# Performance work log

Measured on AMD Instinct MI355X. Metric: run time of the kernel, lower is better.

The kernel has to match this reference:

```python
import jax, jax.numpy as jnp
import numpy as np

H = 16  # num_heads
B, N, M, D = 4, 512, 2048, 1024
FF = 4096  # mlp_ratio * D
LN_EPS = 1e-5


def _ln(x, g, b):
    m = x.mean(-1, keepdims=True)
    v = ((x - m) ** 2).mean(-1, keepdims=True)
    return (x - m) * jax.lax.rsqrt(v + LN_EPS) * g + b


def _attn(q_in, k_in, v_in, wq, bq, wk, bk, wv, bv, wp, bp):
    b, n, d = q_in.shape
    m = k_in.shape[1]
    hd = d // H
    scale = hd ** -0.5
    q = (q_in @ wq + bq).reshape(b, n, H, hd) * scale
    k = (k_in @ wk + bk).reshape(b, m, H, hd)
    v = (v_in @ wv + bv).reshape(b, m, H, hd)
    attn = jax.nn.softmax(jnp.einsum('bnhd,bmhd->bhnm', q, k), axis=-1)
    out = jnp.einsum('bhnm,bmhd->bnhd', attn, v).reshape(b, n, d)
    return out @ wp + bp


def setup_inputs() -> dict:
    key = jax.random.key(0)
    ks = iter(jax.random.split(key, 32))
    rnd = lambda shape: jax.random.normal(next(ks), shape, dtype=jnp.float32)
    w = lambda *shape: rnd(shape) * 0.02
    inp = {
        'state': rnd((B, N, D)),
        'patches': rnd((B, M, D)),
        'patches_pos_embed': rnd((B, M, D)),
        'state_query': rnd((B, N, D)),
    }
    for p in ('ca', 'sa'):
        inp[f'{p}_wq'] = w(D, D); inp[f'{p}_bq'] = jnp.zeros((D,), jnp.float32)
        inp[f'{p}_wk'] = w(D, D); inp[f'{p}_bk'] = jnp.zeros((D,), jnp.float32)
        inp[f'{p}_wv'] = w(D, D); inp[f'{p}_bv'] = jnp.zeros((D,), jnp.float32)
        inp[f'{p}_wp'] = w(D, D); inp[f'{p}_bp'] = jnp.zeros((D,), jnp.float32)
    inp['w1'] = w(D, FF); inp['b1'] = jnp.zeros((FF,), jnp.float32)
    inp['w2'] = w(FF, D); inp['b2'] = jnp.zeros((D,), jnp.float32)
    for i in (1, 2, 3):
        inp[f'n{i}_g'] = jnp.ones((D,), jnp.float32)
        inp[f'n{i}_b'] = jnp.zeros((D,), jnp.float32)
        inp[f'ls{i}'] = jnp.full((D,), 1e-5, jnp.float32)
    return inp


def reference(state, patches, patches_pos_embed, state_query,
              ca_wq, ca_bq, ca_wk, ca_bk, ca_wv, ca_bv, ca_wp, ca_bp,
              sa_wq, sa_bq, sa_wk, sa_bk, sa_wv, sa_bv, sa_wp, sa_bp,
              w1, b1, w2, b2,
              n1_g, n1_b, n2_g, n2_b, n3_g, n3_b,
              ls1, ls2, ls3):
    # pre-norm path of TransformerLayer.forward_pre (dropouts/drop_path = 0)
    state = state + state_query
    kv = patches + patches_pos_embed
    cross = _attn(_ln(state, n1_g, n1_b), kv, patches,
                  ca_wq, ca_bq, ca_wk, ca_bk, ca_wv, ca_bv, ca_wp, ca_bp)
    state = state + cross * ls1
    ns = _ln(state, n2_g, n2_b)
    selfa = _attn(ns, ns, ns,
                  sa_wq, sa_bq, sa_wk, sa_bk, sa_wv, sa_bv, sa_wp, sa_bp)
    state = state + selfa * ls2
    h = jax.nn.gelu(_ln(state, n3_g, n3_b) @ w1 + b1)
    return state + (h @ w2 + b2) * ls3
```

## Files before the change

### kernel.cpp

```cpp
#include <hip/hip_runtime.h>

#define DEV __device__ __forceinline__

typedef __bf16 bf16x8 __attribute__((ext_vector_type(8)));
typedef float f32x4 __attribute__((ext_vector_type(4)));

DEV unsigned short f2bf(float f) {
  __bf16 h = (__bf16)f;
  return __builtin_bit_cast(unsigned short, h);
}
DEV unsigned int cvtpk(float lo, float hi) {
  unsigned int r;
  asm("v_cvt_pk_bf16_f32 %0, %1, %2" : "=v"(r) : "v"(lo), "v"(hi));
  return r;
}

DEV void gload16(const void* g, void* l) {
  __builtin_amdgcn_global_load_lds(
      (const __attribute__((address_space(1))) unsigned int*)g,
      (__attribute__((address_space(3))) unsigned int*)l, 16, 0, 0);
}

DEV void tconv64_body(const float* __restrict__ W, unsigned short* __restrict__ Wt,
                      int K, int N, int bx, int by) {
  __shared__ float tile[64][65];
  const int t = threadIdx.x;
  const int rr = t >> 4;
  const int cc = (t & 15) * 4;
#pragma unroll
  for (int it = 0; it < 4; it++) {
    float4 v = *reinterpret_cast<const float4*>(
        &W[(size_t)(by * 64 + it * 16 + rr) * N + bx * 64 + cc]);
    tile[it * 16 + rr][cc] = v.x;
    tile[it * 16 + rr][cc + 1] = v.y;
    tile[it * 16 + rr][cc + 2] = v.z;
    tile[it * 16 + rr][cc + 3] = v.w;
  }
  __syncthreads();
  const int nr = t >> 3;
  const int kc = (t & 7) * 8;
#pragma unroll
  for (int it = 0; it < 2; it++) {
    const int n = it * 32 + nr;
    uint4 o;
    o.x = cvtpk(tile[kc + 0][n], tile[kc + 1][n]);
    o.y = cvtpk(tile[kc + 2][n], tile[kc + 3][n]);
    o.z = cvtpk(tile[kc + 4][n], tile[kc + 5][n]);
    o.w = cvtpk(tile[kc + 6][n], tile[kc + 7][n]);
    *reinterpret_cast<uint4*>(&Wt[(size_t)(bx * 64 + n) * K + by * 64 + kc]) = o;
  }
}

DEV void add_ln_body(const float* __restrict__ a, const float* b, float* x0_out,
                     unsigned short* __restrict__ y, const float* __restrict__ gam,
                     const float* __restrict__ bet, int row) {
  const int t = threadIdx.x;
  const int c = t * 4;
  const size_t base = (size_t)row * 1024 + c;
  float4 v = *reinterpret_cast<const float4*>(a + base);
  if (b) {
    float4 v2 = *reinterpret_cast<const float4*>(b + base);
    v.x += v2.x; v.y += v2.y; v.z += v2.z; v.w += v2.w;
  }
  if (x0_out) *reinterpret_cast<float4*>(x0_out + base) = v;
  float s = v.x + v.y + v.z + v.w;
  float sq = v.x * v.x + v.y * v.y + v.z * v.z + v.w * v.w;
#pragma unroll
  for (int o = 32; o > 0; o >>= 1) {
    s += __shfl_xor(s, o);
    sq += __shfl_xor(sq, o);
  }
  __shared__ float ps[4], pq[4];
  const int w = t >> 6;
  if ((t & 63) == 0) { ps[w] = s; pq[w] = sq; }
  __syncthreads();
  s = ps[0] + ps[1] + ps[2] + ps[3];
  sq = pq[0] + pq[1] + pq[2] + pq[3];
  const float mean = s * (1.f / 1024.f);
  const float var = sq * (1.f / 1024.f) - mean * mean;
  const float rstd = rsqrtf(var + 1e-5f);
  float4 gv = *reinterpret_cast<const float4*>(gam + c);
  float4 bv = *reinterpret_cast<const float4*>(bet + c);
  uint2 o2;
  o2.x = cvtpk((v.x - mean) * rstd * gv.x + bv.x, (v.y - mean) * rstd * gv.y + bv.y);
  o2.y = cvtpk((v.z - mean) * rstd * gv.z + bv.z, (v.w - mean) * rstd * gv.w + bv.w);
  *reinterpret_cast<uint2*>(y + base) = o2;
}

DEV void kvcast_body4(const float* __restrict__ p, const float* __restrict__ pe,
                      unsigned short* __restrict__ kvo, unsigned short* __restrict__ po,
                      int bid) {
  float4 a[4], b[4];
  size_t idx[4];
#pragma unroll
  for (int it = 0; it < 4; it++) {
    idx[it] = ((size_t)bid * 256 + threadIdx.x + (size_t)it * 524288) * 4;
    a[it] = *reinterpret_cast<const float4*>(p + idx[it]);
    b[it] = *reinterpret_cast<const float4*>(pe + idx[it]);
  }
#pragma unroll
  for (int it = 0; it < 4; it++) {
    uint2 kv2, p2;
    kv2.x = cvtpk(a[it].x + b[it].x, a[it].y + b[it].y);
    kv2.y = cvtpk(a[it].z + b[it].z, a[it].w + b[it].w);
    p2.x = cvtpk(a[it].x, a[it].y);
    p2.y = cvtpk(a[it].z, a[it].w);
    *reinterpret_cast<uint2*>(kvo + idx[it]) = kv2;
    *reinterpret_cast<uint2*>(po + idx[it]) = p2;
  }
}

struct Pre {
  const float* sqw[8]; unsigned short* sqd[8];
  const float* w1; unsigned short* w1t;
  const float* w2; unsigned short* w2t;
  const float* state; const float* squery; float* stateF; unsigned short* lnB;
  const float* n1_g; const float* n1_b;
  const float* patches; const float* ppe; unsigned short* kvB; unsigned short* patB;
  const float* bq; const float* bk; const float* bv; float* bqkv;
};
__global__ __launch_bounds__(256) void prelude_kernel(Pre p) {
  const int bid = blockIdx.x;
  if (bid < 2048) {
    kvcast_body4(p.patches, p.ppe, p.kvB, p.patB, bid);
  } else if (bid < 4096) {
    const int i = bid - 2048;
    const int m = i >> 8, wi = i & 255;
    tconv64_body(p.sqw[m], p.sqd[m], 1024, 1024, wi & 15, wi >> 4);
  } else if (bid < 5120) {
    const int i = bid - 4096;
    tconv64_body(p.w1, p.w1t, 1024, 4096, i & 63, i >> 6);
  } else if (bid < 6144) {
    const int i = bid - 5120;
    tconv64_body(p.w2, p.w2t, 4096, 1024, i & 15, i >> 4);
  } else if (bid < 8192) {
    add_ln_body(p.state, p.squery, p.stateF, p.lnB, p.n1_g, p.n1_b, bid - 6144);
  } else {
    const int i = (bid - 8192) * 256 + threadIdx.x;
    p.bqkv[i] = i < 1024 ? p.bq[i] : (i < 2048 ? p.bk[i - 1024] : p.bv[i - 2048]);
  }
}

__global__ __launch_bounds__(256) void add_ln_kernel(
    const float* __restrict__ a, const float* b, float* x0_out,
    unsigned short* __restrict__ y, const float* __restrict__ gam,
    const float* __restrict__ bet) {
  add_ln_body(a, b, x0_out, y, gam, bet, blockIdx.x);
}

DEV void xcd_swizzle(int gx, int gy, int& bx, int& by, int& bz) {
  const int gxy = gx * gy;
  const int nwg = gxy * gridDim.z;
  const int orig = (blockIdx.z * gy + blockIdx.y) * gx + blockIdx.x;
  const int q = nwg >> 3, r = nwg & 7;
  const int xcd = orig & 7;
  int wgid = (xcd < r ? xcd * (q + 1) : r * (q + 1) + (xcd - r) * q) + (orig >> 3);
  bz = wgid / gxy;
  wgid -= bz * gxy;
  if (gy >= gx) { by = wgid / gx; bx = wgid - by * gx; }
  else          { bx = wgid / gy; by = wgid - bx * gy; }
}

template <int BM, int BN>
DEV void gemm_core(const unsigned short* __restrict__ A,
                   const unsigned short* __restrict__ Bt,
                   unsigned short* As, unsigned short* Bs,
                   int brow, int bcol, int K, int lda, int koff,
                   f32x4 (&acc)[BM / 32][BN / 32]) {
  constexpr int WM = BM / 32, WN = BN / 32;
  const int t = threadIdx.x;
  const int lane = t & 63, w = t >> 6;
  const int wr = w >> 1, wc = w & 1;
  const int g = lane >> 4, lr = lane & 15;
  const int srow = lane >> 2, scol = (lane & 3) * 8;

  auto stage = [&](int buf, int k0) {
#pragma unroll
    for (int i = 0; i < BM / 64; i++) {
      const int r0 = (i * 4 + w) * 16;
      gload16(A + (size_t)(brow + r0 + srow) * lda + koff + k0 + scol,
              &As[buf * BM * 32 + r0 * 32]);
    }
#pragma unroll
    for (int i = 0; i < BN / 64; i++) {
      const int r0 = (i * 4 + w) * 16;
      gload16(Bt + (size_t)(bcol + r0 + srow) * lda + koff + k0 + scol,
              &Bs[buf * BN * 32 + r0 * 32]);
    }
  };

  stage(0, 0);
  const int nk = K / 32;
  int cur = 0;
  for (int kt = 0; kt < nk; kt++) {
    __syncthreads();
    if (kt + 1 < nk) stage(cur ^ 1, (kt + 1) * 32);
    bf16x8 af[WM], bfr[WN];
#pragma unroll
    for (int m = 0; m < WM; m++)
      af[m] = *reinterpret_cast<const bf16x8*>(
          &As[cur * BM * 32 + (wr * (BM / 2) + m * 16 + lr) * 32 + g * 8]);
#pragma unroll
    for (int n = 0; n < WN; n++)
      bfr[n] = *reinterpret_cast<const bf16x8*>(
          &Bs[cur * BN * 32 + (wc * (BN / 2) + n * 16 + lr) * 32 + g * 8]);
    __builtin_amdgcn_s_setprio(1);
#pragma unroll
    for (int m = 0; m < WM; m++)
#pragma unroll
      for (int n = 0; n < WN; n++)
        acc[m][n] = __builtin_amdgcn_mfma_f32_16x16x32_bf16(af[m], bfr[n], acc[m][n], 0, 0, 0);
    __builtin_amdgcn_s_setprio(0);
    cur ^= 1;
  }
}

template <int BM, int BN>
DEV void epilogue_vT(f32x4 (&acc)[BM / 32][BN / 32], unsigned short* smem,
                     unsigned short* __restrict__ vT, const float* __restrict__ bias,
                     int brow, int bcol, int vcol0, int vNk, int rpb) {
  constexpr int WM = BM / 32, WN = BN / 32;
  constexpr int LDT = 136;
  const int t = threadIdx.x, lane = t & 63, w = t >> 6;
  const int wr = w >> 1, wc = w & 1;
  const int g = lane >> 4, lr = lane & 15;
  __syncthreads();
#pragma unroll
  for (int m = 0; m < WM; m++) {
    const int row0 = wr * (BM / 2) + m * 16 + g * 4;
#pragma unroll
    for (int n = 0; n < WN; n++) {
      const int cc = wc * (BN / 2) + n * 16 + lr;
      const float bv = bias[bcol + cc];
      uint2 pk;
      pk.x = cvtpk(acc[m][n][0] + bv, acc[m][n][1] + bv);
      pk.y = cvtpk(acc[m][n][2] + bv, acc[m][n][3] + bv);
      *reinterpret_cast<uint2*>(&smem[cc * LDT + row0]) = pk;
    }
  }
  __syncthreads();
  const int b = brow / rpb;
  const int kvb = brow % rpb;
  constexpr int ITERS = BM * BN / (256 * 8);
#pragma unroll
  for (int it = 0; it < ITERS; it++) {
    const int idx = it * 256 + t;
    const int cc = idx / (BM / 8);
    const int ch = idx % (BM / 8);
    const int dg = bcol + cc - vcol0;
    const int h = dg >> 6, d = dg & 63;
    uint4 v = *reinterpret_cast<uint4*>(&smem[cc * LDT + ch * 8]);
    *reinterpret_cast<uint4*>(
        &vT[((size_t)(b * 16 + h) * 64 + d) * vNk + kvb + ch * 8]) = v;
  }
}

template <int EPI, int BM, int BN>
__global__ __launch_bounds__(256) void gemm_kernel(
    const unsigned short* __restrict__ A, const unsigned short* __restrict__ Bt,
    const float* __restrict__ bias, const float* resid,
    const float* __restrict__ ls, void* outp, int M, int N, int K, int lda,
    unsigned short* vT, int vcol0, int vNk, int rpb) {
  constexpr int WM = BM / 32;
  constexpr int WN = BN / 32;
  constexpr int STG = 2 * BM * 32 + 2 * BN * 32;
  constexpr int TRN = BN * 136;
  constexpr int SME = (EPI == 5 && TRN > STG) ? TRN : STG;
  __shared__ __align__(16) unsigned short smem[SME];
  unsigned short* As = smem;
  unsigned short* Bs = smem + 2 * BM * 32;
  const int t = threadIdx.x;
  const int lane = t & 63, w = t >> 6;
  const int wr = w >> 1, wc = w & 1;
  const int g = lane >> 4, lr = lane & 15;

  int bx, by, bz;
  xcd_swizzle(gridDim.x, gridDim.y, bx, by, bz);
  const int brow = by * BM, bcol = bx * BN;

  f32x4 acc[WM][WN] = {};
  gemm_core<BM, BN>(A, Bt, As, Bs, brow, bcol, K, lda, bz * K, acc);

  if (EPI == 5 && bcol >= vcol0) {
    epilogue_vT<BM, BN>(acc, smem, vT, bias, brow, bcol, vcol0, vNk, rpb);
    return;
  }

#pragma unroll
  for (int m = 0; m < WM; m++) {
    const int row0 = brow + wr * (BM / 2) + m * 16 + g * 4;
#pragma unroll
    for (int n = 0; n < WN; n++) {
      const int col = bcol + wc * (BN / 2) + n * 16 + lr;
      const float bv = (EPI == 4) ? 0.f : bias[col];
#pragma unroll
      for (int r = 0; r < 4; r++) {
        const float v = acc[m][n][r] + bv;
        const size_t idx = (size_t)(row0 + r) * N + col;
        if (EPI == 0 || EPI == 5) {
          ((unsigned short*)outp)[idx] = f2bf(v);
        } else if (EPI == 2) {
          ((float*)outp)[idx] = resid[idx] + v * ls[col];
        } else if (EPI == 3) {
          const float tth = tanhf(0.7978845608028654f * (v + 0.044715f * v * v * v));
          ((unsigned short*)outp)[idx] = f2bf(0.5f * v * (1.f + tth));
        } else {
          ((float*)outp)[(size_t)bz * M * N + idx] = v;
        }
      }
    }
  }
}

struct G3 {
  const unsigned short* A[3]; const unsigned short* Bt[3];
  const float* bias[3]; unsigned short* out[3]; int ecum[3];
  unsigned short* vT; int vNk; int rpb;
};
__global__ __launch_bounds__(256) void gemm3_kernel(G3 p, int N, int K) {
  constexpr int BM = 128, BN = 128, WM = BM / 32, WN = BN / 32;
  constexpr int STG = 2 * BM * 32 + 2 * BN * 32;
  constexpr int TRN = BN * 136;
  constexpr int SME = (TRN > STG) ? TRN : STG;
  __shared__ __align__(16) unsigned short smem[SME];
  unsigned short* As = smem;
  unsigned short* Bs = smem + 2 * BM * 32;
  const int t = threadIdx.x;
  const int lane = t & 63, w = t >> 6;
  const int wr = w >> 1, wc = w & 1;
  const int g = lane >> 4, lr = lane & 15;

  int bx, by, bz;
  xcd_swizzle(gridDim.x, gridDim.y, bx, by, bz);
  const int s = (by >= p.ecum[0]) + (by >= p.ecum[1]);
  const int byloc = by - (s ? p.ecum[s - 1] : 0);
  const unsigned short* A = p.A[s];
  const unsigned short* Bt = p.Bt[s];
  const float* bias = p.bias[s];
  const int brow = byloc * BM, bcol = bx * BN;

  f32x4 acc[WM][WN] = {};
  gemm_core<BM, BN>(A, Bt, As, Bs, brow, bcol, K, K, 0, acc);

  if (s == 2) {
    epilogue_vT<BM, BN>(acc, smem, p.vT, bias, brow, bcol, 0, p.vNk, p.rpb);
    return;
  }
  unsigned short* outp = p.out[s];
#pragma unroll
  for (int m = 0; m < WM; m++) {
    const int row0 = brow + wr * (BM / 2) + m * 16 + g * 4;
#pragma unroll
    for (int n = 0; n < WN; n++) {
      const int col = bcol + wc * (BN / 2) + n * 16 + lr;
      const float bv = bias[col];
#pragma unroll
      for (int r = 0; r < 4; r++)
        outp[(size_t)(row0 + r) * N + col] = f2bf(acc[m][n][r] + bv);
    }
  }
}

__global__ __launch_bounds__(256) void splitk_red_kernel(
    const float* __restrict__ p, const float* __restrict__ bias,
    const float* __restrict__ resid, const float* __restrict__ ls,
    float* __restrict__ out) {
  const size_t i = ((size_t)blockIdx.x * 256 + threadIdx.x) * 4;
  const int c = (int)(i & 1023);
  float4 a = *reinterpret_cast<const float4*>(p + i);
  float4 b = *reinterpret_cast<const float4*>(p + 2048ull * 1024 + i);
  float4 rv = *reinterpret_cast<const float4*>(resid + i);
  float4 bb = *reinterpret_cast<const float4*>(bias + c);
  float4 lv = *reinterpret_cast<const float4*>(ls + c);
  float4 o;
  o.x = rv.x + (a.x + b.x + bb.x) * lv.x;
  o.y = rv.y + (a.y + b.y + bb.y) * lv.y;
  o.z = rv.z + (a.z + b.z + bb.z) * lv.z;
  o.w = rv.w + (a.w + b.w + bb.w) * lv.w;
  *reinterpret_cast<float4*>(out + i) = o;
}

__global__ __launch_bounds__(512) void attn_kernel(
    const unsigned short* __restrict__ Q, const unsigned short* __restrict__ Kp,
    const unsigned short* __restrict__ vT, unsigned short* __restrict__ O,
    int RSq, int RSk, int Nq, int Nk, float k2) {
  __shared__ __align__(16) unsigned short Ks[2][128 * 72];
  __shared__ __align__(16) unsigned short Vs[64 * 136];
  __shared__ __align__(16) unsigned short Ps[128 * 72];
  const int t = threadIdx.x, lane = t & 63, w = t >> 6;
  const int qt = blockIdx.y, h = blockIdx.x & 15, b = blockIdx.x >> 4;
  const int g = lane >> 4, lr = lane & 15;
  const int ksrow = t >> 2, kscol = (t & 3) * 16;
  const int vsrow = t >> 3, vscol = (t & 7) * 16;

  uint4 qr[2];
  {
    const unsigned short* qp = Q + (size_t)(b * Nq + qt * 128 + w * 16 + lr) * RSq + h * 64 + g * 8;
    qr[0] = *reinterpret_cast<const uint4*>(qp);
    qr[1] = *reinterpret_cast<const uint4*>(qp + 32);
  }
  float m_i = -1e30f, l_i = 0.f;
  f32x4 acc_o[4] = {};

  auto kaddr = [&](int kv0) {
    return reinterpret_cast<const uint4*>(
        Kp + (size_t)(b * Nk + kv0 + ksrow) * RSk + h * 64 + kscol);
  };
  auto vaddr = [&](int kv0) {
    return reinterpret_cast<const uint4*>(
        vT + ((size_t)(b * 16 + h) * 64 + vsrow) * Nk + kv0 + vscol);
  };

  uint4 kr0 = kaddr(0)[0], kr1 = kaddr(0)[1];
  uint4 vr0 = vaddr(0)[0], vr1 = vaddr(0)[1];

  int cur = 0;
  for (int kv0 = 0; kv0 < Nk; kv0 += 128) {
    *reinterpret_cast<uint4*>(&Ks[cur][ksrow * 72 + kscol]) = kr0;
    *reinterpret_cast<uint4*>(&Ks[cur][ksrow * 72 + kscol + 8]) = kr1;
    *reinterpret_cast<uint4*>(&Vs[vsrow * 136 + vscol]) = vr0;
    *reinterpret_cast<uint4*>(&Vs[vsrow * 136 + vscol + 8]) = vr1;
    __syncthreads();
    if (kv0 + 128 < Nk) {
      kr0 = kaddr(kv0 + 128)[0]; kr1 = kaddr(kv0 + 128)[1];
      vr0 = vaddr(kv0 + 128)[0]; vr1 = vaddr(kv0 + 128)[1];
    }

    f32x4 accs[8] = {};
    __builtin_amdgcn_s_setprio(1);
#pragma unroll
    for (int d0 = 0; d0 < 64; d0 += 32) {
      bf16x8 qf = __builtin_bit_cast(bf16x8, qr[d0 >> 5]);
#pragma unroll
      for (int m = 0; m < 8; m++) {
        bf16x8 kf = *reinterpret_cast<const bf16x8*>(&Ks[cur][(m * 16 + lr) * 72 + d0 + g * 8]);
        accs[m] = __builtin_amdgcn_mfma_f32_16x16x32_bf16(kf, qf, accs[m], 0, 0, 0);
      }
    }
    __builtin_amdgcn_s_setprio(0);
    float pmax = -1e30f;
#pragma unroll
    for (int m = 0; m < 8; m++)
#pragma unroll
      for (int r = 0; r < 4; r++) pmax = fmaxf(pmax, accs[m][r]);
    pmax = fmaxf(pmax, __shfl_xor(pmax, 16));
    pmax = fmaxf(pmax, __shfl_xor(pmax, 32));
    const float pm2 = pmax * k2;
    if (!__all(pm2 <= m_i + 8.f)) {
      const float m_new = fmaxf(m_i, pm2);
      const float corr = exp2f(m_i - m_new);
      m_i = m_new;
      l_i *= corr;
#pragma unroll
      for (int r = 0; r < 4; r++) {
        const float cf = __shfl(corr, g * 4 + r);
#pragma unroll
        for (int n = 0; n < 4; n++) acc_o[n][r] *= cf;
      }
    }
    float psum = 0.f;
    uint2 pk4[4];
#pragma unroll
    for (int m = 0; m < 8; m++) {
      float p0 = exp2f(fmaf(accs[m][0], k2, -m_i));
      float p1 = exp2f(fmaf(accs[m][1], k2, -m_i));
      float p2 = exp2f(fmaf(accs[m][2], k2, -m_i));
      float p3 = exp2f(fmaf(accs[m][3], k2, -m_i));
      psum += p0 + p1 + p2 + p3;
      uint2 pk;
      pk.x = cvtpk(p0, p1);
      pk.y = cvtpk(p2, p3);
      if (m < 4)
        *reinterpret_cast<uint2*>(&Ps[(w * 16 + lr) * 72 + m * 16 + g * 4]) = pk;
      else
        pk4[m - 4] = pk;
    }
    psum += __shfl_xor(psum, 16);
    psum += __shfl_xor(psum, 32);
    l_i += psum;
    __builtin_amdgcn_s_setprio(1);
#pragma unroll
    for (int ks = 0; ks < 2; ks++) {
      bf16x8 pf = *reinterpret_cast<const bf16x8*>(&Ps[(w * 16 + lr) * 72 + ks * 32 + g * 8]);
#pragma unroll
      for (int n = 0; n < 4; n++) {
        bf16x8 vf = *reinterpret_cast<const bf16x8*>(&Vs[(n * 16 + lr) * 136 + ks * 32 + g * 8]);
        acc_o[n] = __builtin_amdgcn_mfma_f32_16x16x32_bf16(pf, vf, acc_o[n], 0, 0, 0);
      }
    }
    __builtin_amdgcn_s_setprio(0);
#pragma unroll
    for (int m = 0; m < 4; m++)
      *reinterpret_cast<uint2*>(&Ps[(w * 16 + lr) * 72 + m * 16 + g * 4]) = pk4[m];
    __builtin_amdgcn_s_setprio(1);
#pragma unroll
    for (int ks = 2; ks < 4; ks++) {
      bf16x8 pf = *reinterpret_cast<const bf16x8*>(&Ps[(w * 16 + lr) * 72 + (ks - 2) * 32 + g * 8]);
#pragma unroll
      for (int n = 0; n < 4; n++) {
        bf16x8 vf = *reinterpret_cast<const bf16x8*>(&Vs[(n * 16 + lr) * 136 + ks * 32 + g * 8]);
        acc_o[n] = __builtin_amdgcn_mfma_f32_16x16x32_bf16(pf, vf, acc_o[n], 0, 0, 0);
      }
    }
    __builtin_amdgcn_s_setprio(0);
    __syncthreads();
    cur ^= 1;
  }
#pragma unroll
  for (int r = 0; r < 4; r++) {
    const float li = __shfl(l_i, g * 4 + r);
    const float inv = 1.f / li;
    const int qrow = qt * 128 + w * 16 + g * 4 + r;
#pragma unroll
    for (int n = 0; n < 4; n++)
      O[(size_t)(b * Nq + qrow) * 1024 + h * 64 + n * 16 + lr] = f2bf(acc_o[n][r] * inv);
  }
}

extern "C" void kernel_launch(void* const* d_in, const int* in_sizes, int n_in,
                              void* d_out, int out_size, void* d_ws, size_t ws_size,
                              hipStream_t stream) {
  const float* state = (const float*)d_in[0];
  const float* patches = (const float*)d_in[1];
  const float* ppe = (const float*)d_in[2];
  const float* squery = (const float*)d_in[3];
  const float* ca_wq = (const float*)d_in[4];
  const float* ca_bq = (const float*)d_in[5];
  const float* ca_wk = (const float*)d_in[6];
  const float* ca_bk = (const float*)d_in[7];
  const float* ca_wv = (const float*)d_in[8];
  const float* ca_bv = (const float*)d_in[9];
  const float* ca_wp = (const float*)d_in[10];
  const float* ca_bp = (const float*)d_in[11];
  const float* sa_wq = (const float*)d_in[12];
  const float* sa_bq = (const float*)d_in[13];
  const float* sa_wk = (const float*)d_in[14];
  const float* sa_bk = (const float*)d_in[15];
  const float* sa_wv = (const float*)d_in[16];
  const float* sa_bv = (const float*)d_in[17];
  const float* sa_wp = (const float*)d_in[18];
  const float* sa_bp = (const float*)d_in[19];
  const float* w1 = (const float*)d_in[20];
  const float* b1 = (const float*)d_in[21];
  const float* w2 = (const float*)d_in[22];
  const float* b2 = (const float*)d_in[23];
  const float* n1_g = (const float*)d_in[24];
  const float* n1_b = (const float*)d_in[25];
  const float* ls1 = (const float*)d_in[26];
  const float* n2_g = (const float*)d_in[27];
  const float* n2_b = (const float*)d_in[28];
  const float* ls2 = (const float*)d_in[29];
  const float* n3_g = (const float*)d_in[30];
  const float* n3_b = (const float*)d_in[31];
  const float* ls3 = (const float*)d_in[32];

  char* wsp = (char*)d_ws;
  auto alloc = [&](size_t bytes) {
    void* p = (void*)wsp;
    wsp += (bytes + 255) & ~(size_t)255;
    return p;
  };
  float* stateF = (float*)alloc(2048ull * 1024 * 4);
  unsigned short* lnB = (unsigned short*)alloc(2048ull * 1024 * 2);
  unsigned short* kvB = (unsigned short*)alloc(8192ull * 1024 * 2);
  unsigned short* patB = (unsigned short*)alloc(8192ull * 1024 * 2);
  unsigned short* qB = (unsigned short*)alloc(2048ull * 1024 * 2);
  unsigned short* kB = (unsigned short*)alloc(8192ull * 1024 * 2);
  unsigned short* vB = (unsigned short*)alloc(8192ull * 1024 * 2);
  unsigned short* oB = (unsigned short*)alloc(2048ull * 1024 * 2);
  unsigned short* hB = kvB;
  unsigned short* qkvB = kB;
  unsigned short* vTc = vB;
  unsigned short* vTs = qB;
  float* mlp2p = (float*)patB;
  unsigned short* ca_wqt = (unsigned short*)alloc(1024ull * 1024 * 2);
  unsigned short* ca_wkt = (unsigned short*)alloc(1024ull * 1024 * 2);
  unsigned short* ca_wvt = (unsigned short*)alloc(1024ull * 1024 * 2);
  unsigned short* ca_wpt = (unsigned short*)alloc(1024ull * 1024 * 2);
  unsigned short* sa_wqkvt = (unsigned short*)alloc(3072ull * 1024 * 2);
  unsigned short* sa_wpt = (unsigned short*)alloc(1024ull * 1024 * 2);
  unsigned short* w1t = (unsigned short*)alloc(4096ull * 1024 * 2);
  unsigned short* w2t = (unsigned short*)alloc(4096ull * 1024 * 2);
  float* sa_bqkv = (float*)alloc(3072 * 4);

  Pre pre;
  pre.sqw[0] = ca_wq; pre.sqd[0] = ca_wqt;
  pre.sqw[1] = ca_wk; pre.sqd[1] = ca_wkt;
  pre.sqw[2] = ca_wv; pre.sqd[2] = ca_wvt;
  pre.sqw[3] = ca_wp; pre.sqd[3] = ca_wpt;
  pre.sqw[4] = sa_wq; pre.sqd[4] = sa_wqkvt;
  pre.sqw[5] = sa_wk; pre.sqd[5] = sa_wqkvt + 1024ull * 1024;
  pre.sqw[6] = sa_wv; pre.sqd[6] = sa_wqkvt + 2048ull * 1024;
  pre.sqw[7] = sa_wp; pre.sqd[7] = sa_wpt;
  pre.w1 = w1; pre.w1t = w1t; pre.w2 = w2; pre.w2t = w2t;
  pre.state = state; pre.squery = squery; pre.stateF = stateF; pre.lnB = lnB;
  pre.n1_g = n1_g; pre.n1_b = n1_b;
  pre.patches = patches; pre.ppe = ppe; pre.kvB = kvB; pre.patB = patB;
  pre.bq = sa_bq; pre.bk = sa_bk; pre.bv = sa_bv; pre.bqkv = sa_bqkv;
  prelude_kernel<<<8204, 256, 0, stream>>>(pre);

  const float k2 = 0.125f * 1.4426950408889634f;

  G3 g3;
  g3.A[0] = lnB;  g3.Bt[0] = ca_wqt; g3.bias[0] = ca_bq; g3.out[0] = qB;      g3.ecum[0] = 16;
  g3.A[1] = kvB;  g3.Bt[1] = ca_wkt; g3.bias[1] = ca_bk; g3.out[1] = kB;      g3.ecum[1] = 80;
  g3.A[2] = patB; g3.Bt[2] = ca_wvt; g3.bias[2] = ca_bv; g3.out[2] = nullptr; g3.ecum[2] = 144;
  g3.vT = vTc; g3.vNk = 2048; g3.rpb = 2048;
  gemm3_kernel<<<dim3(8, 144), 256, 0, stream>>>(g3, 1024, 1024);
  attn_kernel<<<dim3(64, 4), 512, 0, stream>>>(qB, kB, vTc, oB, 1024, 1024, 512, 2048, k2);
  gemm_kernel<2, 64, 64><<<dim3(16, 32), 256, 0, stream>>>(oB, ca_wpt, ca_bp, stateF, ls1, stateF, 2048, 1024, 1024, 1024, nullptr, 0, 0, 0);

  add_ln_kernel<<<2048, 256, 0, stream>>>(stateF, nullptr, nullptr, lnB, n2_g, n2_b);
  gemm_kernel<5, 128, 64><<<dim3(48, 16), 256, 0, stream>>>(lnB, sa_wqkvt, sa_bqkv, nullptr, nullptr, qkvB, 2048, 3072, 1024, 1024, vTs, 2048, 512, 512);
  attn_kernel<<<dim3(64, 4), 512, 0, stream>>>(qkvB, qkvB + 1024, vTs, oB, 3072, 3072, 512, 512, k2);
  gemm_kernel<2, 64, 64><<<dim3(16, 32), 256, 0, stream>>>(oB, sa_wpt, sa_bp, stateF, ls2, stateF, 2048, 1024, 1024, 1024, nullptr, 0, 0, 0);

  add_ln_kernel<<<2048, 256, 0, stream>>>(stateF, nullptr, nullptr, lnB, n3_g, n3_b);
  gemm_kernel<3, 128, 128><<<dim3(32, 16), 256, 0, stream>>>(lnB, w1t, b1, nullptr, nullptr, hB, 2048, 4096, 1024, 1024, nullptr, 0, 0, 0);
  gemm_kernel<4, 128, 64><<<dim3(16, 16, 2), 256, 0, stream>>>(hB, w2t, nullptr, nullptr, nullptr, mlp2p, 2048, 1024, 2048, 4096, nullptr, 0, 0, 0);
  splitk_red_kernel<<<2048, 256, 0, stream>>>(mlp2p, b2, stateF, ls3, (float*)d_out);
}
```

Measured before the change: 287.6 us.

## Overlap weight transposes with first GEMM and double-buffer V in attention

Only the cross-attention Q/K/V weight transposes stay in the prelude kernel. The remaining transposes (ca_wp, self-attention QKV/proj, w1, w2) and the bias concatenation move into extra blocks of the fused QKV GEMM launch, so they run alongside GEMM tiles instead of ahead of them. Separately, the attention kernel double-buffers the V tile and widens the P buffer to cover the full 128-wide block. This removes the split two-phase P write/read and the trailing per-iteration __syncthreads. The cost is more LDS per attention block and a hand-rolled 1D XCD mapping in the GEMM.

```diff
diff --git a/kernel.cpp b/kernel.cpp
--- a/kernel.cpp
+++ b/kernel.cpp
@@ -22,8 +22,7 @@
 }
 
 DEV void tconv64_body(const float* __restrict__ W, unsigned short* __restrict__ Wt,
-                      int K, int N, int bx, int by) {
-  __shared__ float tile[64][65];
+                      int K, int N, int bx, int by, float* tile ) {
   const int t = threadIdx.x;
   const int rr = t >> 4;
   const int cc = (t & 15) * 4;
@@ -31,10 +30,10 @@
   for (int it = 0; it < 4; it++) {
     float4 v = *reinterpret_cast<const float4*>(
         &W[(size_t)(by * 64 + it * 16 + rr) * N + bx * 64 + cc]);
-    tile[it * 16 + rr][cc] = v.x;
-    tile[it * 16 + rr][cc + 1] = v.y;
-    tile[it * 16 + rr][cc + 2] = v.z;
-    tile[it * 16 + rr][cc + 3] = v.w;
+    tile[(it * 16 + rr) * 65 + cc] = v.x;
+    tile[(it * 16 + rr) * 65 + cc + 1] = v.y;
+    tile[(it * 16 + rr) * 65 + cc + 2] = v.z;
+    tile[(it * 16 + rr) * 65 + cc + 3] = v.w;
   }
   __syncthreads();
   const int nr = t >> 3;
@@ -43,10 +42,10 @@
   for (int it = 0; it < 2; it++) {
     const int n = it * 32 + nr;
     uint4 o;
-    o.x = cvtpk(tile[kc + 0][n], tile[kc + 1][n]);
-    o.y = cvtpk(tile[kc + 2][n], tile[kc + 3][n]);
-    o.z = cvtpk(tile[kc + 4][n], tile[kc + 5][n]);
-    o.w = cvtpk(tile[kc + 6][n], tile[kc + 7][n]);
+    o.x = cvtpk(tile[(kc + 0) * 65 + n], tile[(kc + 1) * 65 + n]);
+    o.y = cvtpk(tile[(kc + 2) * 65 + n], tile[(kc + 3) * 65 + n]);
+    o.z = cvtpk(tile[(kc + 4) * 65 + n], tile[(kc + 5) * 65 + n]);
+    o.w = cvtpk(tile[(kc + 6) * 65 + n], tile[(kc + 7) * 65 + n]);
     *reinterpret_cast<uint4*>(&Wt[(size_t)(bx * 64 + n) * K + by * 64 + kc]) = o;
   }
 }
@@ -111,33 +110,22 @@
 }
 
 struct Pre {
-  const float* sqw[8]; unsigned short* sqd[8];
-  const float* w1; unsigned short* w1t;
-  const float* w2; unsigned short* w2t;
+  const float* caw[3]; unsigned short* cad[3];
   const float* state; const float* squery; float* stateF; unsigned short* lnB;
   const float* n1_g; const float* n1_b;
   const float* patches; const float* ppe; unsigned short* kvB; unsigned short* patB;
-  const float* bq; const float* bk; const float* bv; float* bqkv;
 };
 __global__ __launch_bounds__(256) void prelude_kernel(Pre p) {
+  __shared__ __align__(16) float tile[64 * 65];
   const int bid = blockIdx.x;
   if (bid < 2048) {
     kvcast_body4(p.patches, p.ppe, p.kvB, p.patB, bid);
-  } else if (bid < 4096) {
+  } else if (bid < 2816) {
     const int i = bid - 2048;
     const int m = i >> 8, wi = i & 255;
-    tconv64_body(p.sqw[m], p.sqd[m], 1024, 1024, wi & 15, wi >> 4);
-  } else if (bid < 5120) {
-    const int i = bid - 4096;
-    tconv64_body(p.w1, p.w1t, 1024, 4096, i & 63, i >> 6);
-  } else if (bid < 6144) {
-    const int i = bid - 5120;
-    tconv64_body(p.w2, p.w2t, 4096, 1024, i & 15, i >> 4);
-  } else if (bid < 8192) {
-    add_ln_body(p.state, p.squery, p.stateF, p.lnB, p.n1_g, p.n1_b, bid - 6144);
+    tconv64_body(p.caw[m], p.cad[m], 1024, 1024, wi & 15, wi >> 4, tile);
   } else {
-    const int i = (bid - 8192) * 256 + threadIdx.x;
-    p.bqkv[i] = i < 1024 ? p.bq[i] : (i < 2048 ? p.bk[i - 1024] : p.bv[i - 2048]);
+    add_ln_body(p.state, p.squery, p.stateF, p.lnB, p.n1_g, p.n1_b, bid - 2816);
   }
 }
 
@@ -312,26 +300,55 @@
   }
 }
 
-struct G3 {
+struct G3X {
   const unsigned short* A[3]; const unsigned short* Bt[3];
   const float* bias[3]; unsigned short* out[3]; int ecum[3];
   unsigned short* vT; int vNk; int rpb;
+  const float* wp; unsigned short* wpt;
+  const float* saw[4]; unsigned short* sad[4];
+  const float* w1; unsigned short* w1t;
+  const float* w2; unsigned short* w2t;
+  const float* bq; const float* bk; const float* bv; float* bqkv;
 };
-__global__ __launch_bounds__(256) void gemm3_kernel(G3 p, int N, int K) {
+__global__ __launch_bounds__(256) void gemm3_kernel(G3X p, int N, int K) {
   constexpr int BM = 128, BN = 128, WM = BM / 32, WN = BN / 32;
   constexpr int STG = 2 * BM * 32 + 2 * BN * 32;
   constexpr int TRN = BN * 136;
   constexpr int SME = (TRN > STG) ? TRN : STG;
+  constexpr int NG = 1152;
   __shared__ __align__(16) unsigned short smem[SME];
+  const int bid = blockIdx.x;
+  const int t = threadIdx.x;
+
+  if (bid >= NG) {
+    float* tile = reinterpret_cast<float*>(smem);
+    int i = bid - NG;
+    if (i < 256) {
+      tconv64_body(p.wp, p.wpt, 1024, 1024, i & 15, i >> 4, tile);
+    } else if (i < 1280) {
+      i -= 256;
+      const int m = i >> 8, wi = i & 255;
+      tconv64_body(p.saw[m], p.sad[m], 1024, 1024, wi & 15, wi >> 4, tile);
+    } else if (i < 2304) {
+      i -= 1280;
+      tconv64_body(p.w1, p.w1t, 1024, 4096, i & 63, i >> 6, tile);
+    } else if (i < 3328) {
+      i -= 2304;
+      tconv64_body(p.w2, p.w2t, 4096, 1024, i & 15, i >> 4, tile);
+    } else {
+      const int j = (i - 3328) * 256 + t;
+      p.bqkv[j] = j < 1024 ? p.bq[j] : (j < 2048 ? p.bk[j - 1024] : p.bv[j - 2048]);
+    }
+    return;
+  }
+
   unsigned short* As = smem;
   unsigned short* Bs = smem + 2 * BM * 32;
-  const int t = threadIdx.x;
   const int lane = t & 63, w = t >> 6;
   const int wr = w >> 1, wc = w & 1;
   const int g = lane >> 4, lr = lane & 15;
-
-  int bx, by, bz;
-  xcd_swizzle(gridDim.x, gridDim.y, bx, by, bz);
+  const int wgid = (bid & 7) * (NG >> 3) + (bid >> 3);
+  const int by = wgid >> 3, bx = wgid & 7;
   const int s = (by >= p.ecum[0]) + (by >= p.ecum[1]);
   const int byloc = by - (s ? p.ecum[s - 1] : 0);
   const unsigned short* A = p.A[s];
@@ -385,8 +402,8 @@
     const unsigned short* __restrict__ vT, unsigned short* __restrict__ O,
     int RSq, int RSk, int Nq, int Nk, float k2) {
   __shared__ __align__(16) unsigned short Ks[2][128 * 72];
-  __shared__ __align__(16) unsigned short Vs[64 * 136];
-  __shared__ __align__(16) unsigned short Ps[128 * 72];
+  __shared__ __align__(16) unsigned short Vs[2][64 * 136];
+  __shared__ __align__(16) unsigned short Ps[128 * 136];
   const int t = threadIdx.x, lane = t & 63, w = t >> 6;
   const int qt = blockIdx.y, h = blockIdx.x & 15, b = blockIdx.x >> 4;
   const int g = lane >> 4, lr = lane & 15;
@@ -418,8 +435,8 @@
   for (int kv0 = 0; kv0 < Nk; kv0 += 128) {
     *reinterpret_cast<uint4*>(&Ks[cur][ksrow * 72 + kscol]) = kr0;
     *reinterpret_cast<uint4*>(&Ks[cur][ksrow * 72 + kscol + 8]) = kr1;
-    *reinterpret_cast<uint4*>(&Vs[vsrow * 136 + vscol]) = vr0;
-    *reinterpret_cast<uint4*>(&Vs[vsrow * 136 + vscol + 8]) = vr1;
+    *reinterpret_cast<uint4*>(&Vs[cur][vsrow * 136 + vscol]) = vr0;
+    *reinterpret_cast<uint4*>(&Vs[cur][vsrow * 136 + vscol + 8]) = vr1;
     __syncthreads();
     if (kv0 + 128 < Nk) {
       kr0 = kaddr(kv0 + 128)[0]; kr1 = kaddr(kv0 + 128)[1];
@@ -459,7 +476,6 @@
       }
     }
     float psum = 0.f;
-    uint2 pk4[4];
 #pragma unroll
     for (int m = 0; m < 8; m++) {
       float p0 = exp2f(fmaf(accs[m][0], k2, -m_i));
@@ -470,40 +486,22 @@
       uint2 pk;
       pk.x = cvtpk(p0, p1);
       pk.y = cvtpk(p2, p3);
-      if (m < 4)
-        *reinterpret_cast<uint2*>(&Ps[(w * 16 + lr) * 72 + m * 16 + g * 4]) = pk;
-      else
-        pk4[m - 4] = pk;
+      *reinterpret_cast<uint2*>(&Ps[(w * 16 + lr) * 136 + m * 16 + g * 4]) = pk;
     }
     psum += __shfl_xor(psum, 16);
     psum += __shfl_xor(psum, 32);
     l_i += psum;
     __builtin_amdgcn_s_setprio(1);
 #pragma unroll
-    for (int ks = 0; ks < 2; ks++) {
-      bf16x8 pf = *reinterpret_cast<const bf16x8*>(&Ps[(w * 16 + lr) * 72 + ks * 32 + g * 8]);
+    for (int ks = 0; ks < 4; ks++) {
+      bf16x8 pf = *reinterpret_cast<const bf16x8*>(&Ps[(w * 16 + lr) * 136 + ks * 32 + g * 8]);
 #pragma unroll
       for (int n = 0; n < 4; n++) {
-        bf16x8 vf = *reinterpret_cast<const bf16x8*>(&Vs[(n * 16 + lr) * 136 + ks * 32 + g * 8]);
+        bf16x8 vf = *reinterpret_cast<const bf16x8*>(&Vs[cur][(n * 16 + lr) * 136 + ks * 32 + g * 8]);
         acc_o[n] = __builtin_amdgcn_mfma_f32_16x16x32_bf16(pf, vf, acc_o[n], 0, 0, 0);
       }
     }
     __builtin_amdgcn_s_setprio(0);
-#pragma unroll
-    for (int m = 0; m < 4; m++)
-      *reinterpret_cast<uint2*>(&Ps[(w * 16 + lr) * 72 + m * 16 + g * 4]) = pk4[m];
-    __builtin_amdgcn_s_setprio(1);
-#pragma unroll
-    for (int ks = 2; ks < 4; ks++) {
-      bf16x8 pf = *reinterpret_cast<const bf16x8*>(&Ps[(w * 16 + lr) * 72 + (ks - 2) * 32 + g * 8]);
-#pragma unroll
-      for (int n = 0; n < 4; n++) {
-        bf16x8 vf = *reinterpret_cast<const bf16x8*>(&Vs[(n * 16 + lr) * 136 + ks * 32 + g * 8]);
-        acc_o[n] = __builtin_amdgcn_mfma_f32_16x16x32_bf16(pf, vf, acc_o[n], 0, 0, 0);
-      }
-    }
-    __builtin_amdgcn_s_setprio(0);
-    __syncthreads();
     cur ^= 1;
   }
 #pragma unroll
@@ -584,29 +582,29 @@
   float* sa_bqkv = (float*)alloc(3072 * 4);
 
   Pre pre;
-  pre.sqw[0] = ca_wq; pre.sqd[0] = ca_wqt;
-  pre.sqw[1] = ca_wk; pre.sqd[1] = ca_wkt;
-  pre.sqw[2] = ca_wv; pre.sqd[2] = ca_wvt;
-  pre.sqw[3] = ca_wp; pre.sqd[3] = ca_wpt;
-  pre.sqw[4] = sa_wq; pre.sqd[4] = sa_wqkvt;
-  pre.sqw[5] = sa_wk; pre.sqd[5] = sa_wqkvt + 1024ull * 1024;
-  pre.sqw[6] = sa_wv; pre.sqd[6] = sa_wqkvt + 2048ull * 1024;
-  pre.sqw[7] = sa_wp; pre.sqd[7] = sa_wpt;
-  pre.w1 = w1; pre.w1t = w1t; pre.w2 = w2; pre.w2t = w2t;
+  pre.caw[0] = ca_wq; pre.cad[0] = ca_wqt;
+  pre.caw[1] = ca_wk; pre.cad[1] = ca_wkt;
+  pre.caw[2] = ca_wv; pre.cad[2] = ca_wvt;
   pre.state = state; pre.squery = squery; pre.stateF = stateF; pre.lnB = lnB;
   pre.n1_g = n1_g; pre.n1_b = n1_b;
   pre.patches = patches; pre.ppe = ppe; pre.kvB = kvB; pre.patB = patB;
-  pre.bq = sa_bq; pre.bk = sa_bk; pre.bv = sa_bv; pre.bqkv = sa_bqkv;
-  prelude_kernel<<<8204, 256, 0, stream>>>(pre);
+  prelude_kernel<<<4864, 256, 0, stream>>>(pre);
 
   const float k2 = 0.125f * 1.4426950408889634f;
 
-  G3 g3;
+  G3X g3;
   g3.A[0] = lnB;  g3.Bt[0] = ca_wqt; g3.bias[0] = ca_bq; g3.out[0] = qB;      g3.ecum[0] = 16;
   g3.A[1] = kvB;  g3.Bt[1] = ca_wkt; g3.bias[1] = ca_bk; g3.out[1] = kB;      g3.ecum[1] = 80;
   g3.A[2] = patB; g3.Bt[2] = ca_wvt; g3.bias[2] = ca_bv; g3.out[2] = nullptr; g3.ecum[2] = 144;
   g3.vT = vTc; g3.vNk = 2048; g3.rpb = 2048;
-  gemm3_kernel<<<dim3(8, 144), 256, 0, stream>>>(g3, 1024, 1024);
+  g3.wp = ca_wp; g3.wpt = ca_wpt;
+  g3.saw[0] = sa_wq; g3.sad[0] = sa_wqkvt;
+  g3.saw[1] = sa_wk; g3.sad[1] = sa_wqkvt + 1024ull * 1024;
+  g3.saw[2] = sa_wv; g3.sad[2] = sa_wqkvt + 2048ull * 1024;
+  g3.saw[3] = sa_wp; g3.sad[3] = sa_wpt;
+  g3.w1 = w1; g3.w1t = w1t; g3.w2 = w2; g3.w2t = w2t;
+  g3.bq = sa_bq; g3.bk = sa_bk; g3.bv = sa_bv; g3.bqkv = sa_bqkv;
+  gemm3_kernel<<<4492, 256, 0, stream>>>(g3, 1024, 1024);
   attn_kernel<<<dim3(64, 4), 512, 0, stream>>>(qB, kB, vTc, oB, 1024, 1024, 512, 2048, k2);
   gemm_kernel<2, 64, 64><<<dim3(16, 32), 256, 0, stream>>>(oB, ca_wpt, ca_bp, stateF, ls1, stateF, 2048, 1024, 1024, 1024, nullptr, 0, 0, 0);
 
```

New measurement: 280.3 us. 1.03x faster.
